# Kernel optimization log

Measured on AMD Instinct MI355X. Metric: run time of the kernel, lower is better.

The kernel has to match this reference:

```python
import jax, jax.numpy as jnp
from jax import lax
import numpy as np

NUM_PWMS = 512
FILTER_SIZE = 19
INPUT_LENGTH = 1000
BATCH = 128
SCORING = 'max'


def setup_inputs() -> dict:
    key = jax.random.key(0)
    k1, k2 = jax.random.split(key)
    x = jax.random.normal(k1, (BATCH, 4, INPUT_LENGTH), dtype=jnp.float32)
    pwms = jax.random.normal(k2, (NUM_PWMS, 4, FILTER_SIZE), dtype=jnp.float32)
    return {"x": x, "pwms": pwms}


def _pwm_scan(x, pwms):
    # Grouped conv with groups=num_pwms over x.repeat(1, num_pwms, 1) is
    # mathematically identical to a plain cross-correlation of every PWM
    # against the 4-channel input (each group sees the same 4 channels).
    # lax conv performs cross-correlation, matching torch.nn.Conv1d.
    dn = lax.conv_dimension_numbers(x.shape, pwms.shape, ('NCH', 'OIH', 'NCH'))
    return lax.conv_general_dilated(x, pwms, (1,), 'VALID', dimension_numbers=dn)


def reference(x, pwms):
    # forward strand scores: [B, num_pwms, L - filter + 1]
    o = _pwm_scan(x, pwms)
    # reverse complement: flip channel (complement base) and length axes
    x_rev = x[:, ::-1, ::-1]
    o_rev = _pwm_scan(x_rev, pwms)
    o = jnp.concatenate((o, o_rev), axis=2)  # [B, num_pwms, 2*(L-f+1)]
    if SCORING == 'max':
        return jnp.max(o, axis=2)
    else:
        return jnp.sum(o, axis=2)
```

## Files before the change

kernel.cpp:

```cpp
#include <hip/hip_runtime.h>
#include <math.h>

#define BATCH 128
#define NPWM 512
#define LEN 1000
#define NEXT 1024
#define KSLOT 96

typedef _Float16 f16x4 __attribute__((ext_vector_type(4)));
typedef _Float16 f16x8 __attribute__((ext_vector_type(8)));
typedef float    f32x4 __attribute__((ext_vector_type(4)));

#define MFMA16(a, b, c) __builtin_amdgcn_mfma_f32_16x16x32_f16(a, b, c, 0, 0, 0)

__global__ __launch_bounds__(256)
void prepack_w(const float* __restrict__ w, _Float16* __restrict__ wf)
{
    int idx = blockIdx.x * 256 + threadIdx.x;
    if (idx >= NEXT * KSLOT) return;
    int fe = idx / KSLOT;
    int t  = idx - fe * KSLOT;
    int kk = t >> 2;
    int c  = t & 3;
    int f      = fe >> 1;
    int strand = fe & 1;
    float v = 0.0f;
    if (kk < 19)
        v = strand ? w[f*76 + (3-c)*19 + (18-kk)]
                   : w[f*76 + c*19 + kk];
    wf[idx] = (_Float16)v;
}

#define LDB(EO) __extension__ ({                                         \
    f16x4 p0_ = *(const f16x4*)(H + (EO));                               \
    f16x4 p1_ = *(const f16x4*)(H + (EO) + 4);                           \
    __builtin_shufflevector(p0_, p1_, 0,1,2,3,4,5,6,7); })

__global__ __launch_bounds__(256)
void pwm_mfma(const float* __restrict__ x,
              const _Float16* __restrict__ wf,
              float* __restrict__ out)
{
    __shared__ __align__(16) _Float16 H[4096];
    __shared__ float red[128];

    const int tid   = threadIdx.x;
    const int b     = blockIdx.x;
    const int ftile = blockIdx.y;
    const int lane  = tid & 63;
    const int wave  = tid >> 6;
    const int row   = lane & 15;
    const int g     = lane >> 4;

    for (int i = tid; i < 1024; i += 256) {
        f16x4 hv;
        #pragma unroll
        for (int c = 0; c < 4; ++c) {
            float v = (i < LEN) ? x[(size_t)b*4000 + c*1000 + i] : 0.0f;
            hv[c] = (_Float16)v;
        }
        *(f16x4*)(H + i*4) = hv;
    }

    f16x8 wa[2][3];
    {
        const int f0 = ftile*128 + wave*32;
        #pragma unroll
        for (int fg = 0; fg < 2; ++fg)
            #pragma unroll
            for (int s = 0; s < 3; ++s) {
                const size_t o = (size_t)(f0 + fg*16 + row)*KSLOT + s*32 + g*8;
                wa[fg][s] = *(const f16x8*)(wf + o);
            }
    }
    __syncthreads();

    const int base = row*4 + g*8;
    const f32x4 zc = {};

    float m0[4], m1[4];
    #pragma unroll
    for (int r = 0; r < 4; ++r) { m0[r] = -INFINITY; m1[r] = -INFINITY; }

    for (int it = 0; it < 31; ++it) {
        const int o_ = it*128 + base;
        f16x8 g0 = LDB(o_);
        f16x8 g1 = LDB(o_ + 32);
        f16x8 g2 = LDB(o_ + 64);
        f16x8 g3 = LDB(o_ + 96);
        f16x8 g4 = LDB(o_ + 128);

        f32x4 a00 = MFMA16(wa[0][0], g0, zc);
        f32x4 a10 = MFMA16(wa[1][0], g0, zc);
        f32x4 a01 = MFMA16(wa[0][0], g2, zc);
        f32x4 a11 = MFMA16(wa[1][0], g2, zc);
        a00 = MFMA16(wa[0][1], g1, a00);
        a10 = MFMA16(wa[1][1], g1, a10);
        a01 = MFMA16(wa[0][1], g3, a01);
        a11 = MFMA16(wa[1][1], g3, a11);
        a00 = MFMA16(wa[0][2], g2, a00);
        a10 = MFMA16(wa[1][2], g2, a10);
        a01 = MFMA16(wa[0][2], g4, a01);
        a11 = MFMA16(wa[1][2], g4, a11);

        if (it == 30 && row >= 6) {
            #pragma unroll
            for (int r = 0; r < 4; ++r) { a01[r] = -INFINITY; a11[r] = -INFINITY; }
        }
        #pragma unroll
        for (int r = 0; r < 4; ++r) {
            m0[r] = fmaxf(m0[r], fmaxf(a00[r], a01[r]));
            m1[r] = fmaxf(m1[r], fmaxf(a10[r], a11[r]));
        }
    }

    #pragma unroll
    for (int off = 1; off < 16; off <<= 1)
        #pragma unroll
        for (int r = 0; r < 4; ++r) {
            m0[r] = fmaxf(m0[r], __shfl_xor(m0[r], off, 64));
            m1[r] = fmaxf(m1[r], __shfl_xor(m1[r], off, 64));
        }

    if (row == 0) {
        #pragma unroll
        for (int r = 0; r < 4; ++r) {
            red[wave*32 +      g*4 + r] = m0[r];
            red[wave*32 + 16 + g*4 + r] = m1[r];
        }
    }
    __syncthreads();
    if (tid < 64)
        out[(size_t)b*NPWM + ftile*64 + tid] = fmaxf(red[2*tid], red[2*tid+1]);
}

extern "C" void kernel_launch(void* const* d_in, const int* in_sizes, int n_in,
                              void* d_out, int out_size, void* d_ws, size_t ws_size,
                              hipStream_t stream)
{
    const float* x = (const float*)d_in[0];
    const float* w = (const float*)d_in[1];
    float* out = (float*)d_out;

    _Float16* wf = (_Float16*)d_ws;

    prepack_w<<<dim3((NEXT*KSLOT + 255)/256), 256, 0, stream>>>(w, wf);
    pwm_mfma<<<dim3(BATCH, 8), 256, 0, stream>>>(x, wf, out);
}
```

Baseline: 33.53 us.

## Split waves across sequence halves, each computing 64 filters per B-fragment load

Each wave now covers 64 filter rows (four 16-row groups) instead of 32, over half of the sequence iterations. Pairs of waves split the position range and their partial maxima are merged through a two-slot shared reduction buffer. Every LDS B-fragment load now feeds four MFMAs instead of two, which halves LDS read traffic per MFMA, and loads are interleaved with MFMA issue. The cost is more VGPRs for weights and accumulators, with launch bounds requesting 4 blocks per CU, which risks spills or lower occupancy.

```diff
diff --git a/kernel.cpp b/kernel.cpp
--- a/kernel.cpp
+++ b/kernel.cpp
@@ -36,19 +36,21 @@
     f16x4 p1_ = *(const f16x4*)(H + (EO) + 4);                           \
     __builtin_shufflevector(p0_, p1_, 0,1,2,3,4,5,6,7); })
 
-__global__ __launch_bounds__(256)
+__global__ __launch_bounds__(256, 4)
 void pwm_mfma(const float* __restrict__ x,
               const _Float16* __restrict__ wf,
               float* __restrict__ out)
 {
     __shared__ __align__(16) _Float16 H[4096];
-    __shared__ float red[128];
+    __shared__ float red[2][128];
 
     const int tid   = threadIdx.x;
     const int b     = blockIdx.x;
     const int ftile = blockIdx.y;
     const int lane  = tid & 63;
     const int wave  = tid >> 6;
+    const int fhalf = wave & 1;
+    const int wp    = wave >> 1;
     const int row   = lane & 15;
     const int g     = lane >> 4;
 
@@ -62,11 +64,11 @@
         *(f16x4*)(H + i*4) = hv;
     }
 
-    f16x8 wa[2][3];
+    f16x8 wa[4][3];
     {
-        const int f0 = ftile*128 + wave*32;
+        const int f0 = ftile*128 + fhalf*64;
         #pragma unroll
-        for (int fg = 0; fg < 2; ++fg)
+        for (int fg = 0; fg < 4; ++fg)
             #pragma unroll
             for (int s = 0; s < 3; ++s) {
                 const size_t o = (size_t)(f0 + fg*16 + row)*KSLOT + s*32 + g*8;
@@ -78,60 +80,70 @@
     const int base = row*4 + g*8;
     const f32x4 zc = {};
 
-    float m0[4], m1[4];
+    float m[4][4];
     #pragma unroll
-    for (int r = 0; r < 4; ++r) { m0[r] = -INFINITY; m1[r] = -INFINITY; }
+    for (int fg = 0; fg < 4; ++fg)
+        #pragma unroll
+        for (int r = 0; r < 4; ++r) m[fg][r] = -INFINITY;
 
-    for (int it = 0; it < 31; ++it) {
+    const int it_beg = wp ? 16 : 0;
+    const int it_end = wp ? 31 : 16;
+    for (int it = it_beg; it < it_end; ++it) {
         const int o_ = it*128 + base;
+        f32x4 a0[4], a1[4];
+
         f16x8 g0 = LDB(o_);
+        f16x8 g2 = LDB(o_ + 64);
+        #pragma unroll
+        for (int fg = 0; fg < 4; ++fg) a0[fg] = MFMA16(wa[fg][0], g0, zc);
+        #pragma unroll
+        for (int fg = 0; fg < 4; ++fg) a1[fg] = MFMA16(wa[fg][0], g2, zc);
         f16x8 g1 = LDB(o_ + 32);
-        f16x8 g2 = LDB(o_ + 64);
+        #pragma unroll
+        for (int fg = 0; fg < 4; ++fg) a0[fg] = MFMA16(wa[fg][1], g1, a0[fg]);
         f16x8 g3 = LDB(o_ + 96);
+        #pragma unroll
+        for (int fg = 0; fg < 4; ++fg) a1[fg] = MFMA16(wa[fg][1], g3, a1[fg]);
+        #pragma unroll
+        for (int fg = 0; fg < 4; ++fg) a0[fg] = MFMA16(wa[fg][2], g2, a0[fg]);
         f16x8 g4 = LDB(o_ + 128);
-
-        f32x4 a00 = MFMA16(wa[0][0], g0, zc);
-        f32x4 a10 = MFMA16(wa[1][0], g0, zc);
-        f32x4 a01 = MFMA16(wa[0][0], g2, zc);
-        f32x4 a11 = MFMA16(wa[1][0], g2, zc);
-        a00 = MFMA16(wa[0][1], g1, a00);
-        a10 = MFMA16(wa[1][1], g1, a10);
-        a01 = MFMA16(wa[0][1], g3, a01);
-        a11 = MFMA16(wa[1][1], g3, a11);
-        a00 = MFMA16(wa[0][2], g2, a00);
-        a10 = MFMA16(wa[1][2], g2, a10);
-        a01 = MFMA16(wa[0][2], g4, a01);
-        a11 = MFMA16(wa[1][2], g4, a11);
+        #pragma unroll
+        for (int fg = 0; fg < 4; ++fg) a1[fg] = MFMA16(wa[fg][2], g4, a1[fg]);
 
         if (it == 30 && row >= 6) {
             #pragma unroll
-            for (int r = 0; r < 4; ++r) { a01[r] = -INFINITY; a11[r] = -INFINITY; }
+            for (int fg = 0; fg < 4; ++fg)
+                #pragma unroll
+                for (int r = 0; r < 4; ++r) a1[fg][r] = -INFINITY;
         }
         #pragma unroll
-        for (int r = 0; r < 4; ++r) {
-            m0[r] = fmaxf(m0[r], fmaxf(a00[r], a01[r]));
-            m1[r] = fmaxf(m1[r], fmaxf(a10[r], a11[r]));
-        }
+        for (int fg = 0; fg < 4; ++fg)
+            #pragma unroll
+            for (int r = 0; r < 4; ++r)
+                m[fg][r] = fmaxf(m[fg][r], fmaxf(a0[fg][r], a1[fg][r]));
     }
 
     #pragma unroll
     for (int off = 1; off < 16; off <<= 1)
         #pragma unroll
-        for (int r = 0; r < 4; ++r) {
-            m0[r] = fmaxf(m0[r], __shfl_xor(m0[r], off, 64));
-            m1[r] = fmaxf(m1[r], __shfl_xor(m1[r], off, 64));
-        }
+        for (int fg = 0; fg < 4; ++fg)
+            #pragma unroll
+            for (int r = 0; r < 4; ++r)
+                m[fg][r] = fmaxf(m[fg][r], __shfl_xor(m[fg][r], off, 64));
 
     if (row == 0) {
         #pragma unroll
-        for (int r = 0; r < 4; ++r) {
-            red[wave*32 +      g*4 + r] = m0[r];
-            red[wave*32 + 16 + g*4 + r] = m1[r];
-        }
+        for (int fg = 0; fg < 4; ++fg)
+            #pragma unroll
+            for (int r = 0; r < 4; ++r)
+                red[wp][fhalf*64 + fg*16 + g*4 + r] = m[fg][r];
     }
     __syncthreads();
-    if (tid < 64)
-        out[(size_t)b*NPWM + ftile*64 + tid] = fmaxf(red[2*tid], red[2*tid+1]);
+    if (tid < 64) {
+        float v0 = fmaxf(red[0][2*tid], red[0][2*tid+1]);
+        float v1 = fmaxf(red[1][2*tid], red[1][2*tid+1]);
+        out[(size_t)b*NPWM + ftile*64 + tid] = fmaxf(v0, v1);
+    }
 }
 
 extern "C" void kernel_launch(void* const* d_in, const int* in_sizes, int n_in,
```

New measurement: 31.09 us. 7.3% less time.
